# Optimization experiments

Measured on AMD Instinct MI355X. Metric: run time of the kernel, lower is better.

## Reference

```python
import jax, jax.numpy as jnp
import numpy as np


def bilinear_sample(img, coords):
    # img: [N, H, W] correlation slices; coords: [N, K, K, 2] with (x, y) pixel coords.
    # Matches F.grid_sample(mode='bilinear', padding_mode='zeros', align_corners=True)
    # since the torch bilinear_sampler maps pixel coords to [-1,1] with align_corners=True.
    N, H, W = img.shape
    x = coords[..., 0]
    y = coords[..., 1]
    x0 = jnp.floor(x)
    y0 = jnp.floor(y)
    wx = x - x0  # weight toward x0+1
    wy = y - y0  # weight toward y0+1
    flat = img.reshape(N, H * W)

    def gather(yi, xi):
        valid = (xi >= 0) & (xi <= W - 1) & (yi >= 0) & (yi <= H - 1)
        xi_c = jnp.clip(xi, 0, W - 1).astype(jnp.int32)
        yi_c = jnp.clip(yi, 0, H - 1).astype(jnp.int32)
        idx = (yi_c * W + xi_c).reshape(N, -1)
        vals = jnp.take_along_axis(flat, idx, axis=1).reshape(xi.shape)
        return jnp.where(valid, vals, jnp.zeros((), img.dtype))

    v00 = gather(y0, x0)
    v01 = gather(y0, x0 + 1)
    v10 = gather(y0 + 1, x0)
    v11 = gather(y0 + 1, x0 + 1)
    return (v00 * (1 - wy) * (1 - wx) + v01 * (1 - wy) * wx
            + v10 * wy * (1 - wx) + v11 * wy * wx)


def corr_block(fmap1, fmap2, coords, num_levels, radius):
    B, D, H, W = fmap1.shape
    f1 = fmap1.reshape(B, D, H * W)
    f2 = fmap2.reshape(B, D, H * W)
    # [B, H1*W1, H2*W2] correlation volume, scaled by 1/sqrt(dim)
    corr = jnp.einsum('bdn,bdm->bnm', f1, f2) / jnp.sqrt(jnp.asarray(D, jnp.float32))
    corr = corr.reshape(B * H * W, H, W)

    pyramid = [corr]
    for _ in range(num_levels - 1):
        n, h, w = corr.shape
        # avg_pool2d(kernel=2, stride=2)
        corr = corr.reshape(n, h // 2, 2, w // 2, 2).mean(axis=(2, 4))
        pyramid.append(corr)

    r = radius
    d = jnp.linspace(-r, r, 2 * r + 1, dtype=jnp.float32)
    # meshgrid(dy, dx) stacked on last dim -> delta[...,0]=dy, delta[...,1]=dx
    delta = jnp.stack(jnp.meshgrid(d, d, indexing='ij'), axis=-1)  # [2r+1, 2r+1, 2]

    coords_q = coords.transpose(0, 2, 3, 1).reshape(B * H * W, 1, 1, 2)
    outs = []
    for i, c in enumerate(pyramid):
        coords_lvl = coords_q / (2 ** i) + delta[None]  # [N, 2r+1, 2r+1, 2]
        sampled = bilinear_sample(c, coords_lvl)        # [N, 2r+1, 2r+1]
        outs.append(sampled.reshape(B, H, W, -1))
    out = jnp.concatenate(outs, axis=-1)  # [B, H, W, num_levels*(2r+1)^2]
    return out.transpose(0, 3, 1, 2).astype(jnp.float32)


def setup_inputs() -> dict:
    key = jax.random.key(0)
    k1, k2, k3 = jax.random.split(key, 3)
    B, D, H, W = 4, 256, 64, 64
    fmap1 = jax.random.normal(k1, (B, D, H, W), dtype=jnp.float32)
    fmap2 = jax.random.normal(k2, (B, D, H, W), dtype=jnp.float32)
    coords = jax.random.uniform(k3, (B, 2, H, W), dtype=jnp.float32) * (W - 1)
    return {"fmap1": fmap1, "fmap2": fmap2, "coords": coords,
            "num_levels": 4, "radius": 4}


def reference(fmap1, fmap2, coords, num_levels, radius):
    return corr_block(fmap1, fmap2, coords, num_levels, radius)
```

## Files before the change

### kernel.cpp

```cpp
#include <hip/hip_runtime.h>

typedef unsigned short ushort_t;
typedef __attribute__((ext_vector_type(8))) short bfrag;
typedef __attribute__((ext_vector_type(4))) float f4;

#define NB 4
#define ND 256
#define NH 64
#define NW 64
#define NQ (NH * NW)
#define MPAD 5504
#define NLVL 4
#define NCH (NLVL * 81)

__device__ __forceinline__ float bf2f(ushort_t u) {
    return __uint_as_float(((unsigned)u) << 16);
}
__device__ __forceinline__ ushort_t f2bf(float f) {
    unsigned u = __float_as_uint(f);
    unsigned r = (u + 0x7fffu + ((u >> 16) & 1u)) >> 16;
    return (ushort_t)r;
}

__device__ __forceinline__ void gload_lds16(const void* g, void* l) {
    __builtin_amdgcn_global_load_lds(
        (const __attribute__((address_space(1))) unsigned int*)g,
        (__attribute__((address_space(3))) unsigned int*)l, 16, 0, 0);
}

__global__ __launch_bounds__(256) void pre_kernel(
    const float* __restrict__ f1, const float* __restrict__ f2,
    ushort_t* __restrict__ Abf, ushort_t* __restrict__ Ball)
{
    __shared__ float tile[64][65];
    const int tid = threadIdx.x;
    const int z = blockIdx.z;
    const int b = z & 3;
    const bool isA = (z < 4);
    const float* ib = (isA ? f1 : f2) + (size_t)b * ND * NQ;
    ushort_t* ob = isA ? (Abf + (size_t)b * NQ * ND) : (Ball + (size_t)b * MPAD * ND);
    const float scale = isA ? 0.0625f : 1.0f;
    const int n0 = blockIdx.x * 64, d0 = blockIdx.y * 64;
    const int nl = tid & 63, dg = tid >> 6;
#pragma unroll
    for (int i = 0; i < 16; i++) {
        int dl = dg + i * 4;
        tile[dl][nl] = ib[(size_t)(d0 + dl) * NQ + n0 + nl];
    }
    __syncthreads();
    const int dl = tid & 63, ng = tid >> 6;
#pragma unroll
    for (int i = 0; i < 16; i++) {
        int nn = ng + i * 4;
        ob[(size_t)(n0 + nn) * ND + d0 + dl] = f2bf(tile[dl][nn] * scale);
    }
}

__global__ __launch_bounds__(256) void sort_kernel(
    const float* __restrict__ coords, int* __restrict__ perm)
{
    __shared__ int hist[64];
    __shared__ int base[64];
    const int tid = threadIdx.x;
    const int b   = blockIdx.x;
    if (tid < 64) hist[tid] = 0;
    __syncthreads();
    int keys[16];
#pragma unroll
    for (int i = 0; i < 16; i++) {
        int q = tid + i * 256;
        float cy = coords[((size_t)b * 2 + 1) * NQ + q];
        keys[i] = (int)floorf(cy);
        atomicAdd(&hist[keys[i]], 1);
    }
    __syncthreads();
    if (tid == 0) {
        int s = 0;
        for (int i = 0; i < 64; i++) { base[i] = s; s += hist[i]; }
    }
    __syncthreads();
#pragma unroll
    for (int i = 0; i < 16; i++) {
        int q = tid + i * 256;
        int pos = atomicAdd(&base[keys[i]], 1);
        perm[(size_t)b * NQ + pos] = q;
    }
}

__global__ __launch_bounds__(256) void tbls_kernel(
    const float* __restrict__ coords, const int* __restrict__ perm,
    int* __restrict__ tblS)
{
    const int idx = blockIdx.x * 256 + threadIdx.x;
    const int b = idx >> 12, pos = idx & 4095;
    const int q = perm[(size_t)b * NQ + pos];
    const float cx = coords[((size_t)b * 2 + 0) * NQ + q];
    const float cy = coords[((size_t)b * 2 + 1) * NQ + q];
#pragma unroll
    for (int lvl = 0; lvl < 4; lvl++) {
        float s = 1.0f / (float)(1 << lvl);
        int x0 = (int)floorf(cx * s);
        int y0 = (int)floorf(cy * s);
        tblS[(((size_t)b * 4 + lvl) << 12) + pos] = x0 | (y0 << 6) | (q << 12);
    }
}

__global__ __launch_bounds__(256) void pool_fused(ushort_t* __restrict__ Ball)
{
    const int d = threadIdx.x;
    const int bid = blockIdx.x;
    const int b = bid >> 6;
    const int cell = bid & 63;
    const int Y = cell >> 3, X = cell & 7;
    ushort_t* base = Ball + (size_t)b * MPAD * ND;

    float s1[4][4];
#pragma unroll
    for (int iy = 0; iy < 4; iy++)
#pragma unroll
        for (int ix = 0; ix < 4; ix++) {
            int ry = 2 * (4 * Y + iy), rx = 2 * (4 * X + ix);
            float s = bf2f(base[(size_t)((ry    ) * 64 + rx    ) * ND + d])
                    + bf2f(base[(size_t)((ry    ) * 64 + rx + 1) * ND + d])
                    + bf2f(base[(size_t)((ry + 1) * 64 + rx    ) * ND + d])
                    + bf2f(base[(size_t)((ry + 1) * 64 + rx + 1) * ND + d]);
            s1[iy][ix] = s * 0.25f;
            base[(size_t)(4096 + (4 * Y + iy) * 32 + 4 * X + ix) * ND + d] = f2bf(s1[iy][ix]);
        }
    float s2[2][2];
#pragma unroll
    for (int iy = 0; iy < 2; iy++)
#pragma unroll
        for (int ix = 0; ix < 2; ix++) {
            float s = 0.25f * (s1[2*iy][2*ix] + s1[2*iy][2*ix+1]
                             + s1[2*iy+1][2*ix] + s1[2*iy+1][2*ix+1]);
            s2[iy][ix] = s;
            base[(size_t)(5120 + (2 * Y + iy) * 16 + 2 * X + ix) * ND + d] = f2bf(s);
        }
    float s3 = 0.25f * (s2[0][0] + s2[0][1] + s2[1][0] + s2[1][1]);
    base[(size_t)(5376 + Y * 8 + X) * ND + d] = f2bf(s3);
}

__global__ __launch_bounds__(512, 4) void gemm_corr(
    const ushort_t* __restrict__ A,
    const ushort_t* __restrict__ Bm,
    ushort_t* __restrict__ compact,
    const int* __restrict__ perm,
    const int* __restrict__ tblS)
{
    __shared__ ushort_t As[3][256 * 32];
    __shared__ ushort_t Bs[3][128 * 32];

    const int l   = blockIdx.x;
    const int wg  = (l & 7) * 344 + (l >> 3);
    const int z   = wg / 688;
    const int rem = wg - z * 688;
    const int by  = rem / 43;
    const int bxt = rem - by * 43;

    int lvl, mbase;
    if (bxt < 32)      { lvl = 0; mbase = bxt * 128; }
    else if (bxt < 40) { lvl = 1; mbase = 4096 + (bxt - 32) * 128; }
    else if (bxt < 42) { lvl = 2; mbase = 5120 + (bxt - 40) * 128; }
    else               { lvl = 3; mbase = 5376; }

    const int* tbL = tblS + (((size_t)z * 4 + lvl) << 12);

    if (lvl < 3) {
        int yF = (tbL[by * 256] >> 6) & 63;
        int yL = (tbL[by * 256 + 255] >> 6) & 63;
        int rlo, rhi;
        if (lvl == 0)      { rlo = bxt * 2;        rhi = rlo + 1; }
        else if (lvl == 1) { rlo = (bxt - 32) * 4; rhi = rlo + 3; }
        else               { rlo = (bxt - 40) * 8; rhi = rlo + 7; }
        if (rhi < yF - 4 || rlo > yL + 5) return;
    }

    const int tid  = threadIdx.x;
    const int lane = tid & 63;
    const int wv   = tid >> 6;
    const int wr   = wv >> 1;
    const int wc   = wv & 1;
    const int ln15 = lane & 15;
    const int g4   = lane >> 4;

    const ushort_t* Bb = Bm + ((size_t)z * MPAD + (size_t)mbase) * ND;

    f4 acc[4][4] = {};

    const int rA  = tid >> 2;
    const int chA = (tid & 3) ^ ((tid >> 3) & 3);
    const int* pm = perm + (size_t)z * NQ + by * 256;
    const ushort_t* srcA0 = A + ((size_t)z * NQ + pm[rA])       * ND + chA * 8;
    const ushort_t* srcA1 = A + ((size_t)z * NQ + pm[128 + rA]) * ND + chA * 8;
    const ushort_t* srcB  = Bb + (size_t)rA * ND + chA * 8;

#define STAGE(buf, kk) {                                                   \
    gload_lds16(srcA0 + (kk), &As[buf][tid * 8]);                          \
    gload_lds16(srcA1 + (kk), &As[buf][(512 + tid) * 8]);                  \
    gload_lds16(srcB  + (kk), &Bs[buf][tid * 8]); }

    const int kch = (g4 ^ ((ln15 >> 1) & 3)) * 8;

    STAGE(0, 0);
    STAGE(1, 32);
    STAGE(2, 64);

#pragma unroll
    for (int t = 0; t < 8; ++t) {
        const int cur = t % 3;
        if (t < 6)       { asm volatile("s_waitcnt vmcnt(6)" ::: "memory"); }
        else if (t == 6) { asm volatile("s_waitcnt vmcnt(3)" ::: "memory"); }
        else             { asm volatile("s_waitcnt vmcnt(0)" ::: "memory"); }
        __builtin_amdgcn_s_barrier();
        asm volatile("" ::: "memory");

        bfrag a[4], bb[4];
#pragma unroll
        for (int mi = 0; mi < 4; mi++)
            a[mi] = *reinterpret_cast<const bfrag*>(
                &As[cur][(wr * 64 + mi * 16 + ln15) * 32 + kch]);
#pragma unroll
        for (int ni = 0; ni < 4; ni++)
            bb[ni] = *reinterpret_cast<const bfrag*>(
                &Bs[cur][(wc * 64 + ni * 16 + ln15) * 32 + kch]);

        if (t < 5) {
            __builtin_amdgcn_sched_barrier(0);
            asm volatile("s_waitcnt lgkmcnt(0)" ::: "memory");
            __builtin_amdgcn_s_barrier();
            asm volatile("" ::: "memory");
            STAGE(cur, (t + 3) * 32);
        }

#pragma unroll
        for (int mi = 0; mi < 4; mi++)
#pragma unroll
            for (int ni = 0; ni < 4; ni++)
                acc[mi][ni] = __builtin_amdgcn_mfma_f32_16x16x32_bf16(
                    a[mi], bb[ni], acc[mi][ni], 0, 0, 0);
    }
#undef STAGE

    const int row_base = by * 256 + wr * 64 + (g4 << 2);
    ushort_t* cmp      = compact + (size_t)z * NQ * 400 + lvl * 100;

    auto for_q = [&](auto body) {
#pragma unroll
        for (int mi = 0; mi < 4; mi++) {
            const int q0 = row_base + mi * 16;
            const int4 xy4 = *reinterpret_cast<const int4*>(&tbL[q0]);
            const int xys[4] = {xy4.x, xy4.y, xy4.z, xy4.w};
#pragma unroll
            for (int j = 0; j < 4; j++) {
                const int e = xys[j];
                body(mi, j, e & 63, (e >> 6) & 63, (size_t)((e >> 12) & 4095) * 400);
            }
        }
    };

    if (lvl == 0) {
        const int yfix = bxt * 2 + wc;
        for_q([&](int mi, int j, int x0, int y0, size_t qb) {
            unsigned v = (unsigned)(yfix - y0 + 4);
            if (v < 10u) {
                size_t vb = qb + v * 10;
#pragma unroll
                for (int ni = 0; ni < 4; ni++) {
                    unsigned u = (unsigned)(ln15 + 16 * ni + 4 - x0);
                    if (u < 10u) cmp[vb + u] = f2bf(acc[mi][ni][j]);
                }
            }
        });
    } else if (lvl == 1) {
        const int ybase = (bxt - 32) * 4 + wc * 2;
        for_q([&](int mi, int j, int x0, int y0, size_t qb) {
            unsigned u0 = (unsigned)(ln15 + 4 - x0), u1 = u0 + 16u;
            unsigned v0 = (unsigned)(ybase - y0 + 4), v1 = v0 + 1u;
            if (v0 < 10u) {
                if (u0 < 10u) cmp[qb + v0 * 10 + u0] = f2bf(acc[mi][0][j]);
                if (u1 < 10u) cmp[qb + v0 * 10 + u1] = f2bf(acc[mi][1][j]);
            }
            if (v1 < 10u) {
                if (u0 < 10u) cmp[qb + v1 * 10 + u0] = f2bf(acc[mi][2][j]);
                if (u1 < 10u) cmp[qb + v1 * 10 + u1] = f2bf(acc[mi][3][j]);
            }
        });
    } else if (lvl == 2) {
        const int ybase = (bxt - 40) * 8 + wc * 4;
        for_q([&](int mi, int j, int x0, int y0, size_t qb) {
            unsigned u = (unsigned)(ln15 + 4 - x0);
            if (u < 10u) {
#pragma unroll
                for (int ni = 0; ni < 4; ni++) {
                    unsigned v = (unsigned)(ybase + ni - y0 + 4);
                    if (v < 10u) cmp[qb + v * 10 + u] = f2bf(acc[mi][ni][j]);
                }
            }
        });
    } else if (wc == 0) {
        const int yb3 = ln15 >> 3;
        for_q([&](int mi, int j, int x0, int y0, size_t qb) {
            unsigned u = (unsigned)((ln15 & 7) + 4 - x0);
            if (u < 10u) {
#pragma unroll
                for (int ni = 0; ni < 4; ni++) {
                    unsigned v = (unsigned)(yb3 + 2 * ni - y0 + 4);
                    if (v < 10u) cmp[qb + v * 10 + u] = f2bf(acc[mi][ni][j]);
                }
            }
        });
    }
}

__global__ __launch_bounds__(256) void sample_kernel(
    const ushort_t* __restrict__ compact,
    const float* __restrict__ coords,
    float* __restrict__ out)
{
    __shared__ int   X0s[16], Y0s[16];
    __shared__ float wxs[16], wys[16];
    __shared__ float Dl[16 * 101];
    const int tid = threadIdx.x;
    const int g   = blockIdx.x;
    const int lvl = blockIdx.y;
    const int b   = blockIdx.z;
    const int Wl  = NW >> lvl;

    if (tid < 16) {
        int q = g * 16 + tid;
        float cx = coords[(size_t)(b * 2 + 0) * NQ + q];
        float cy = coords[(size_t)(b * 2 + 1) * NQ + q];
        float s = 1.0f / (float)(1 << lvl);
        float xl = cx * s, yl = cy * s;
        float fx = floorf(xl), fy = floorf(yl);
        X0s[tid] = (int)fx;
        Y0s[tid] = (int)fy;
        wxs[tid] = xl - fx;
        wys[tid] = yl - fy;
    }
    __syncthreads();

#pragma unroll
    for (int r = 0; r < 7; r++) {
        int e = r * 256 + tid;
        if (e < 16 * 100) {
            int qi = e / 100;
            int el = e - qi * 100;
            int v = el / 10;
            int u = el - v * 10;
            int xx = X0s[qi] - 4 + u;
            int yy = Y0s[qi] - 4 + v;
            float val = 0.f;
            if ((unsigned)xx < (unsigned)Wl && (unsigned)yy < (unsigned)Wl)
                val = bf2f(compact[((size_t)b * NQ + g * 16 + qi) * 400
                                   + lvl * 100 + el]);
            Dl[qi * 101 + el] = val;
        }
    }
    __syncthreads();

#pragma unroll
    for (int r = 0; r < 6; r++) {
        int e = r * 256 + tid;
        if (e < 16 * 81) {
            int qi = e & 15;
            int c = e >> 4;
            int i = c / 9;
            int j = c - i * 9;
            float wx = wxs[qi], wy = wys[qi];
            const float* dq = &Dl[qi * 101];
            float d00 = dq[j * 10 + i];
            float d10 = dq[j * 10 + i + 1];
            float d01 = dq[(j + 1) * 10 + i];
            float d11 = dq[(j + 1) * 10 + i + 1];
            float vx0 = d00 + wx * (d10 - d00);
            float vx1 = d01 + wx * (d11 - d01);
            float val = vx0 + wy * (vx1 - vx0);
            out[((size_t)b * NCH + lvl * 81 + c) * NQ + g * 16 + qi] = val;
        }
    }
}

extern "C" void kernel_launch(void* const* d_in, const int* in_sizes, int n_in,
                              void* d_out, int out_size, void* d_ws, size_t ws_size,
                              hipStream_t stream)
{
    const float* fmap1  = (const float*)d_in[0];
    const float* fmap2  = (const float*)d_in[1];
    const float* coords = (const float*)d_in[2];
    float* out = (float*)d_out;

    char* ws = (char*)d_ws;
    const size_t A_BYTES   = (size_t)NB * NQ * ND * 2;
    const size_t B_BYTES   = (size_t)NB * MPAD * ND * 2;
    const size_t CMP_BYTES = (size_t)NB * NQ * 400 * 2;
    const size_t TBL_BYTES = (size_t)NB * 4 * NQ * 4;
    ushort_t* Abf  = (ushort_t*)ws;
    ushort_t* Ball = (ushort_t*)(ws + A_BYTES);
    ushort_t* cmp  = (ushort_t*)(ws + A_BYTES + B_BYTES);
    int*      tblS = (int*)(ws + A_BYTES + B_BYTES + CMP_BYTES);
    int*      perm = (int*)(ws + A_BYTES + B_BYTES + CMP_BYTES + TBL_BYTES);

    pre_kernel<<<dim3(64, 4, 8), 256, 0, stream>>>(fmap1, fmap2, Abf, Ball);

    sort_kernel<<<NB, 256, 0, stream>>>(coords, perm);
    tbls_kernel<<<(NB * NQ) / 256, 256, 0, stream>>>(coords, perm, tblS);

    pool_fused<<<NB * 64, 256, 0, stream>>>(Ball);

    gemm_corr<<<dim3(16 * 43 * NB), 512, 0, stream>>>(Abf, Ball, cmp, perm, tblS);

    sample_kernel<<<dim3(256, NLVL, NB), 256, 0, stream>>>(cmp, coords, out);
}
```

Measured before the change: 67.89 us.

## Fuse sort and table build, scatter A rows in sorted order during transpose

The sort kernel now also builds the per-level lookup table and writes an inverse permutation, so the separate table kernel is removed. The transpose/convert kernel scatters fmap1 rows straight into their sorted positions. The GEMM can then read A tiles contiguously without an index lookup. The serial prefix sum becomes a wavefront shuffle scan. This trades one launch and the indirect loads for a scattered write, and it puts the sort ahead of the conversion kernel.

```diff
diff --git a/kernel.cpp b/kernel.cpp
--- a/kernel.cpp
+++ b/kernel.cpp
@@ -28,8 +28,57 @@
         (__attribute__((address_space(3))) unsigned int*)l, 16, 0, 0);
 }
 
+__global__ __launch_bounds__(256) void sort_kernel(
+    const float* __restrict__ coords,
+    int* __restrict__ inv,
+    int* __restrict__ tblS)
+{
+    __shared__ int hist[64];
+    __shared__ int base[64];
+    const int tid = threadIdx.x;
+    const int b   = blockIdx.x;
+    if (tid < 64) hist[tid] = 0;
+    __syncthreads();
+    int   keys[16];
+    float cxs[16], cys[16];
+#pragma unroll
+    for (int i = 0; i < 16; i++) {
+        int q = tid + i * 256;
+        cxs[i] = coords[((size_t)b * 2 + 0) * NQ + q];
+        cys[i] = coords[((size_t)b * 2 + 1) * NQ + q];
+        keys[i] = (int)floorf(cys[i]);
+        atomicAdd(&hist[keys[i]], 1);
+    }
+    __syncthreads();
+    if (tid < 64) {
+        int v = hist[tid];
+        int s = v;
+#pragma unroll
+        for (int off = 1; off < 64; off <<= 1) {
+            int o = __shfl_up(s, off);
+            if (tid >= off) s += o;
+        }
+        base[tid] = s - v;
+    }
+    __syncthreads();
+#pragma unroll
+    for (int i = 0; i < 16; i++) {
+        int q = tid + i * 256;
+        int pos = atomicAdd(&base[keys[i]], 1);
+        inv[(size_t)b * NQ + q] = pos;
+#pragma unroll
+        for (int lvl = 0; lvl < 4; lvl++) {
+            float s = 1.0f / (float)(1 << lvl);
+            int x0 = (int)floorf(cxs[i] * s);
+            int y0 = (int)floorf(cys[i] * s);
+            tblS[(((size_t)b * 4 + lvl) << 12) + pos] = x0 | (y0 << 6) | (q << 12);
+        }
+    }
+}
+
 __global__ __launch_bounds__(256) void pre_kernel(
     const float* __restrict__ f1, const float* __restrict__ f2,
+    const int* __restrict__ inv,
     ushort_t* __restrict__ Abf, ushort_t* __restrict__ Ball)
 {
     __shared__ float tile[64][65];
@@ -49,59 +98,12 @@
     }
     __syncthreads();
     const int dl = tid & 63, ng = tid >> 6;
+    const int* invb = inv + (size_t)b * NQ;
 #pragma unroll
     for (int i = 0; i < 16; i++) {
         int nn = ng + i * 4;
-        ob[(size_t)(n0 + nn) * ND + d0 + dl] = f2bf(tile[dl][nn] * scale);
-    }
-}
-
-__global__ __launch_bounds__(256) void sort_kernel(
-    const float* __restrict__ coords, int* __restrict__ perm)
-{
-    __shared__ int hist[64];
-    __shared__ int base[64];
-    const int tid = threadIdx.x;
-    const int b   = blockIdx.x;
-    if (tid < 64) hist[tid] = 0;
-    __syncthreads();
-    int keys[16];
-#pragma unroll
-    for (int i = 0; i < 16; i++) {
-        int q = tid + i * 256;
-        float cy = coords[((size_t)b * 2 + 1) * NQ + q];
-        keys[i] = (int)floorf(cy);
-        atomicAdd(&hist[keys[i]], 1);
-    }
-    __syncthreads();
-    if (tid == 0) {
-        int s = 0;
-        for (int i = 0; i < 64; i++) { base[i] = s; s += hist[i]; }
-    }
-    __syncthreads();
-#pragma unroll
-    for (int i = 0; i < 16; i++) {
-        int q = tid + i * 256;
-        int pos = atomicAdd(&base[keys[i]], 1);
-        perm[(size_t)b * NQ + pos] = q;
-    }
-}
-
-__global__ __launch_bounds__(256) void tbls_kernel(
-    const float* __restrict__ coords, const int* __restrict__ perm,
-    int* __restrict__ tblS)
-{
-    const int idx = blockIdx.x * 256 + threadIdx.x;
-    const int b = idx >> 12, pos = idx & 4095;
-    const int q = perm[(size_t)b * NQ + pos];
-    const float cx = coords[((size_t)b * 2 + 0) * NQ + q];
-    const float cy = coords[((size_t)b * 2 + 1) * NQ + q];
-#pragma unroll
-    for (int lvl = 0; lvl < 4; lvl++) {
-        float s = 1.0f / (float)(1 << lvl);
-        int x0 = (int)floorf(cx * s);
-        int y0 = (int)floorf(cy * s);
-        tblS[(((size_t)b * 4 + lvl) << 12) + pos] = x0 | (y0 << 6) | (q << 12);
+        int row = isA ? invb[n0 + nn] : (n0 + nn);
+        ob[(size_t)row * ND + d0 + dl] = f2bf(tile[dl][nn] * scale);
     }
 }
 
@@ -145,7 +147,6 @@
     const ushort_t* __restrict__ A,
     const ushort_t* __restrict__ Bm,
     ushort_t* __restrict__ compact,
-    const int* __restrict__ perm,
     const int* __restrict__ tblS)
 {
     __shared__ ushort_t As[3][256 * 32];
@@ -184,15 +185,15 @@
     const int ln15 = lane & 15;
     const int g4   = lane >> 4;
 
+    const ushort_t* Ab = A  + ((size_t)z * NQ   + (size_t)by * 256) * ND;
     const ushort_t* Bb = Bm + ((size_t)z * MPAD + (size_t)mbase) * ND;
 
     f4 acc[4][4] = {};
 
     const int rA  = tid >> 2;
     const int chA = (tid & 3) ^ ((tid >> 3) & 3);
-    const int* pm = perm + (size_t)z * NQ + by * 256;
-    const ushort_t* srcA0 = A + ((size_t)z * NQ + pm[rA])       * ND + chA * 8;
-    const ushort_t* srcA1 = A + ((size_t)z * NQ + pm[128 + rA]) * ND + chA * 8;
+    const ushort_t* srcA0 = Ab + (size_t)rA * ND + chA * 8;
+    const ushort_t* srcA1 = srcA0 + (size_t)128 * ND;
     const ushort_t* srcB  = Bb + (size_t)rA * ND + chA * 8;
 
 #define STAGE(buf, kk) {                                                   \
@@ -400,16 +401,15 @@
     ushort_t* Ball = (ushort_t*)(ws + A_BYTES);
     ushort_t* cmp  = (ushort_t*)(ws + A_BYTES + B_BYTES);
     int*      tblS = (int*)(ws + A_BYTES + B_BYTES + CMP_BYTES);
-    int*      perm = (int*)(ws + A_BYTES + B_BYTES + CMP_BYTES + TBL_BYTES);
-
-    pre_kernel<<<dim3(64, 4, 8), 256, 0, stream>>>(fmap1, fmap2, Abf, Ball);
-
-    sort_kernel<<<NB, 256, 0, stream>>>(coords, perm);
-    tbls_kernel<<<(NB * NQ) / 256, 256, 0, stream>>>(coords, perm, tblS);
+    int*      inv  = (int*)(ws + A_BYTES + B_BYTES + CMP_BYTES + TBL_BYTES);
+
+    sort_kernel<<<NB, 256, 0, stream>>>(coords, inv, tblS);
+
+    pre_kernel<<<dim3(64, 4, 8), 256, 0, stream>>>(fmap1, fmap2, inv, Abf, Ball);
 
     pool_fused<<<NB * 64, 256, 0, stream>>>(Ball);
 
-    gemm_corr<<<dim3(16 * 43 * NB), 512, 0, stream>>>(Abf, Ball, cmp, perm, tblS);
+    gemm_corr<<<dim3(16 * 43 * NB), 512, 0, stream>>>(Abf, Ball, cmp, tblS);
 
     sample_kernel<<<dim3(256, NLVL, NB), 256, 0, stream>>>(cmp, coords, out);
 }
```

Result: slower. 70.43 us (+3.7%).
